# Performance work log

Measured on AMD Instinct MI355X. Metric: run time of the kernel, lower is better.

## Reference

```python
import math
import jax, jax.numpy as jnp
import numpy as np

H = 32          # num query heads
KVH = 8         # num kv heads
HD = 128        # head dim
THETA = 10000.0
ROT = HD // 2   # 64: source applies RoPE only to first head_dim//2 dims


def setup_inputs() -> dict:
    key = jax.random.key(0)
    ks = jax.random.split(key, 5)
    B, S, D = 1, 2048, 4096
    hidden_states = jax.random.normal(ks[0], (B, S, D), dtype=jnp.float32)
    # additive causal mask: 0 on/below diagonal, large negative above
    causal = jnp.tril(jnp.ones((S, S), dtype=bool))
    attention_mask = jnp.where(causal, 0.0, -1e9).astype(jnp.float32)[None, None]
    position_ids = jnp.arange(S, dtype=jnp.int32)[None, :]
    sc = 1.0 / math.sqrt(D)
    Wq = jax.random.normal(ks[1], (D, H * HD), dtype=jnp.float32) * sc
    Wk = jax.random.normal(ks[2], (D, KVH * HD), dtype=jnp.float32) * sc
    Wv = jax.random.normal(ks[3], (D, KVH * HD), dtype=jnp.float32) * sc
    Wo = jax.random.normal(ks[4], (H * HD, D), dtype=jnp.float32) * sc
    return {"hidden_states": hidden_states, "attention_mask": attention_mask,
            "position_ids": position_ids, "Wq": Wq, "Wk": Wk, "Wv": Wv, "Wo": Wo}


def _rope_cos_sin(position_ids):
    # freqs over HD (head_dim) with step 2 -> ROT=64 frequencies
    freqs = 1.0 / THETA ** (jnp.arange(0, HD, 2, dtype=jnp.float32) / HD)  # [ROT]
    # gather per position: [1, S, ROT] -> broadcast over heads
    ang = position_ids.astype(jnp.float32)[..., None] * freqs             # [1, S, ROT]
    return jnp.cos(ang)[:, None], jnp.sin(ang)[:, None]                    # [1,1,S,ROT]


def _apply_rope(x, cos, sin):
    # x: [B, h, S, HD]; rotate only first ROT dims, splitting that slice in half
    xr = x[..., :ROT]
    x1, x2 = xr[..., : ROT // 2], xr[..., ROT // 2:]
    rot = jnp.concatenate([-x2, x1], axis=-1)
    return jnp.concatenate([xr * cos + rot * sin, x[..., ROT:]], axis=-1)


def reference(hidden_states, attention_mask, position_ids, Wq, Wk, Wv, Wo):
    B, S, D = hidden_states.shape
    q = (hidden_states @ Wq).reshape(B, S, H, HD).transpose(0, 2, 1, 3)      # [B,H,S,HD]
    k = (hidden_states @ Wk).reshape(B, S, KVH, HD).transpose(0, 2, 1, 3)    # [B,KVH,S,HD]
    v = (hidden_states @ Wv).reshape(B, S, KVH, HD).transpose(0, 2, 1, 3)
    cos, sin = _rope_cos_sin(position_ids)
    q = _apply_rope(q, cos, sin)
    k = _apply_rope(k, cos, sin)
    # GQA: repeat kv heads to match query heads
    rep = H // KVH
    k = jnp.repeat(k, rep, axis=1)
    v = jnp.repeat(v, rep, axis=1)
    scores = jnp.einsum('bhqd,bhkd->bhqk', q, k) / math.sqrt(HD)
    scores = scores + attention_mask
    attn = jax.nn.softmax(scores.astype(jnp.float32), axis=-1).astype(q.dtype)
    out = jnp.einsum('bhqk,bhkd->bhqd', attn, v)                              # [B,H,S,HD]
    out = out.transpose(0, 2, 1, 3).reshape(B, S, H * HD)
    return out @ Wo
```

## Files before the change

kernel.cpp:

```cpp
#include <hip/hip_runtime.h>
#include <hip/hip_bf16.h>
#include <stdint.h>

typedef uint16_t u16;
typedef __bf16 bf16x8 __attribute__((ext_vector_type(8)));
typedef float f32x4 __attribute__((ext_vector_type(4)));
typedef u16 u16x4 __attribute__((ext_vector_type(4)));
typedef uint32_t u32x2 __attribute__((ext_vector_type(2)));

#define S_LEN 2048
#define D_MODEL 4096
#define N_HEADS 32
#define N_KVH 8
#define HEAD_DIM 128
#define QD 4096
#define KVD 1024
#define KVS 2048
#define NF  6144

#define QSC 0.1275253958595506f
#define M2F 16.0f

typedef __attribute__((address_space(3))) uint8_t lds_u8;
typedef const __attribute__((address_space(1))) uint8_t glb_u8;

__device__ __forceinline__ float bf2f(u16 x) {
    union { unsigned u; float f; } c; c.u = ((unsigned)x) << 16; return c.f;
}
__device__ __forceinline__ u16 f2bf(float f) {
    union { float f; unsigned u; } c; c.f = f;
    unsigned u = c.u;
    u += 0x7fffu + ((u >> 16) & 1u);
    return (u16)(u >> 16);
}
__device__ __forceinline__ uint32_t cvt_pk_bf16(float a, float b) {
    uint32_t r;
    asm("v_cvt_pk_bf16_f32 %0, %1, %2" : "=v"(r) : "v"(a), "v"(b));
    return r;
}

__global__ __launch_bounds__(256) void conv_f2b_kernel(
    const float* __restrict__ in, u16* __restrict__ out, int n4)
{
    int i = blockIdx.x * blockDim.x + threadIdx.x;
    if (i < n4) {
        float4 v = ((const float4*)in)[i];
        u16x4 o;
        o.x = f2bf(v.x); o.y = f2bf(v.y); o.z = f2bf(v.z); o.w = f2bf(v.w);
        ((u16x4*)out)[i] = o;
    }
}

__global__ __launch_bounds__(256) void transpose_f2b_fast(
    const float* __restrict__ in, u16* __restrict__ out, int R, int C)
{
    __shared__ u16 tile[64 * 70];
    const int cb = blockIdx.x * 64;
    const int rb = blockIdx.y * 64;
    const int t = threadIdx.x;
    const int lr = t >> 4;
    const int lc = (t & 15) * 4;
#pragma unroll
    for (int i = 0; i < 4; ++i) {
        int r = lr + i * 16;
        float4 v = *(const float4*)(in + (size_t)(rb + r) * C + cb + lc);
        u16* d = tile + r * 70 + lc;
        d[0] = f2bf(v.x); d[1] = f2bf(v.y); d[2] = f2bf(v.z); d[3] = f2bf(v.w);
    }
    __syncthreads();
    const int sc = t >> 4;
    const int sr = (t & 15) * 4;
#pragma unroll
    for (int i = 0; i < 4; ++i) {
        int c = sc + i * 16;
        u16x4 o;
        o.x = tile[(sr + 0) * 70 + c];
        o.y = tile[(sr + 1) * 70 + c];
        o.z = tile[(sr + 2) * 70 + c];
        o.w = tile[(sr + 3) * 70 + c];
        *(u16x4*)(out + (size_t)(cb + c) * R + rb + sr) = o;
    }
}

__global__ __launch_bounds__(256) void transpose_b16_fast(
    const u16* __restrict__ in, u16* __restrict__ out, int R, int C, int ld)
{
    __shared__ u16 tile[64 * 70];
    const int cb = blockIdx.x * 64;
    const int rb = blockIdx.y * 64;
    const int t = threadIdx.x;
    const int lr = t >> 4;
    const int lc = (t & 15) * 4;
#pragma unroll
    for (int i = 0; i < 4; ++i) {
        int r = lr + i * 16;
        u16x4 v = *(const u16x4*)(in + (size_t)(rb + r) * ld + cb + lc);
        u16* d = tile + r * 70 + lc;
        d[0] = v.x; d[1] = v.y; d[2] = v.z; d[3] = v.w;
    }
    __syncthreads();
    const int sc = t >> 4;
    const int sr = (t & 15) * 4;
#pragma unroll
    for (int i = 0; i < 4; ++i) {
        int c = sc + i * 16;
        u16x4 o;
        o.x = tile[(sr + 0) * 70 + c];
        o.y = tile[(sr + 1) * 70 + c];
        o.z = tile[(sr + 2) * 70 + c];
        o.w = tile[(sr + 3) * 70 + c];
        *(u16x4*)(out + (size_t)(cb + c) * R + rb + sr) = o;
    }
}

__global__ void rope_table_kernel(const int* __restrict__ pos,
                                  float* __restrict__ ctab, float* __restrict__ stab)
{
    int s = blockIdx.x;
    int i = threadIdx.x;
    float p = (float)pos[s];
    float freq = __expf(-(float)i * (9.210340371976184f / 64.0f));
    float ang = p * freq;
    ctab[s * 64 + i] = cosf(ang);
    stab[s * 64 + i] = sinf(ang);
}

#define BM 128
#define BN 128
#define BKK 64

#define GEMM_PREAMBLE(Nval)                                                    \
    const int K = D_MODEL;                                                     \
    __shared__ u16 sA[2][BM * BKK];                                            \
    __shared__ u16 sB[2][BN * BKK];                                            \
    const int nbx = (Nval) / BN;                                               \
    const int bx = blockIdx.x % nbx;                                           \
    const int by = blockIdx.x / nbx;                                           \
    const int row0 = by * BM, col0 = bx * BN;                                  \
    const int t = threadIdx.x;                                                 \
    const int w = t >> 6, l = t & 63;                                          \
    const int wr = w >> 1, wc = w & 1;                                         \
    const int l16 = l & 15, lk = l >> 4;                                       \
    f32x4 acc[4][4] = {};                                                      \
    auto stage = [&](int buf, int k0) {                                        \
        _Pragma("unroll")                                                      \
        for (int j = 0; j < 4; ++j) {                                          \
            int chunk = j * 256 + w * 64 + l;                                  \
            int r = chunk >> 3;                                                \
            int pc = chunk & 7;                                                \
            int gch = pc ^ (r & 7);                                            \
            const u16* ga = A  + (size_t)(row0 + r) * K + k0 + gch * 8;        \
            const u16* gb = BT + (size_t)(col0 + r) * K + k0 + gch * 8;        \
            __builtin_amdgcn_global_load_lds((glb_u8*)ga,                      \
                (lds_u8*)(sA[buf] + (size_t)(j * 256 + w * 64) * 8), 16, 0, 0);\
            __builtin_amdgcn_global_load_lds((glb_u8*)gb,                      \
                (lds_u8*)(sB[buf] + (size_t)(j * 256 + w * 64) * 8), 16, 0, 0);\
        }                                                                      \
    };                                                                         \
    stage(0, 0);                                                               \
    int cur = 0;                                                               \
    for (int k0 = 0; k0 < K; k0 += BKK) {                                      \
        __syncthreads();                                                       \
        if (k0 + BKK < K) stage(cur ^ 1, k0 + BKK);                            \
        const u16* cA = sA[cur];                                               \
        const u16* cB = sB[cur];                                               \
        _Pragma("unroll")                                                      \
        for (int kk = 0; kk < 2; ++kk) {                                       \
            bf16x8 af[4], bfr[4];                                              \
            _Pragma("unroll")                                                  \
            for (int m = 0; m < 4; ++m) {                                      \
                int r = wr * 64 + m * 16 + l16;                                \
                int ch = (kk * 4 + lk) ^ (r & 7);                              \
                af[m] = *(const bf16x8*)(cA + r * BKK + ch * 8);               \
            }                                                                  \
            _Pragma("unroll")                                                  \
            for (int n = 0; n < 4; ++n) {                                      \
                int r = wc * 64 + n * 16 + l16;                                \
                int ch = (kk * 4 + lk) ^ (r & 7);                              \
                bfr[n] = *(const bf16x8*)(cB + r * BKK + ch * 8);              \
            }                                                                  \
            __builtin_amdgcn_s_setprio(1);                                     \
            _Pragma("unroll")                                                  \
            for (int m = 0; m < 4; ++m)                                        \
                _Pragma("unroll")                                              \
                for (int n = 0; n < 4; ++n)                                    \
                    acc[m][n] = __builtin_amdgcn_mfma_f32_16x16x32_bf16(       \
                        af[m], bfr[n], acc[m][n], 0, 0, 0);                    \
            __builtin_amdgcn_s_setprio(0);                                     \
        }                                                                      \
        cur ^= 1;                                                              \
    }

__global__ __launch_bounds__(256) void gemm_q_kernel(
    const u16* __restrict__ A, const u16* __restrict__ BT, u16* __restrict__ Qm,
    const float* __restrict__ ctab, const float* __restrict__ stab)
{
    GEMM_PREAMBLE(QD)

    const int colbase = col0 + wc * 64;
    const bool doRot = (colbase & 127) == 0;
#pragma unroll
    for (int m = 0; m < 4; ++m) {
        const int rbase = row0 + wr * 64 + m * 16 + lk * 4;
        float vv[4][4];
#pragma unroll
        for (int n = 0; n < 4; ++n)
#pragma unroll
            for (int j = 0; j < 4; ++j) vv[n][j] = acc[m][n][j];
        if (doRot) {
#pragma unroll
            for (int n = 0; n < 2; ++n) {
                int d = n * 16 + l16;
#pragma unroll
                for (int j = 0; j < 4; ++j) {
                    int r = rbase + j;
                    float c1 = ctab[r * 64 + d],      s1 = stab[r * 64 + d];
                    float c2 = ctab[r * 64 + d + 32], s2 = stab[r * 64 + d + 32];
                    float a = vv[n][j], b = vv[n + 2][j];
                    vv[n][j]     = a * c1 - b * s1;
                    vv[n + 2][j] = b * c2 + a * s2;
                }
            }
        }
#pragma unroll
        for (int n = 0; n < 4; ++n)
#pragma unroll
            for (int j = 0; j < 4; ++j)
                Qm[(size_t)(rbase + j) * QD + colbase + n * 16 + l16] =
                    f2bf(vv[n][j] * QSC);
    }
}

__global__ __launch_bounds__(256) void gemm_kv_kernel(
    const u16* __restrict__ A, const u16* __restrict__ BT,
    u16* __restrict__ Km, u16* __restrict__ Vm,
    const float* __restrict__ ctab, const float* __restrict__ stab)
{
    GEMM_PREAMBLE(KVS)

    const int colbase = col0 + wc * 64;
    const bool isK = colbase < KVD;
    const bool doRot = isK && ((colbase & 127) == 0);
#pragma unroll
    for (int m = 0; m < 4; ++m) {
        const int rbase = row0 + wr * 64 + m * 16 + lk * 4;
        float vv[4][4];
#pragma unroll
        for (int n = 0; n < 4; ++n)
#pragma unroll
            for (int j = 0; j < 4; ++j) vv[n][j] = acc[m][n][j];
        if (doRot) {
#pragma unroll
            for (int n = 0; n < 2; ++n) {
                int d = n * 16 + l16;
#pragma unroll
                for (int j = 0; j < 4; ++j) {
                    int r = rbase + j;
                    float c1 = ctab[r * 64 + d],      s1 = stab[r * 64 + d];
                    float c2 = ctab[r * 64 + d + 32], s2 = stab[r * 64 + d + 32];
                    float a = vv[n][j], b = vv[n + 2][j];
                    vv[n][j]     = a * c1 - b * s1;
                    vv[n + 2][j] = b * c2 + a * s2;
                }
            }
        }
        if (isK) {
#pragma unroll
            for (int n = 0; n < 4; ++n)
#pragma unroll
                for (int j = 0; j < 4; ++j)
                    Km[(size_t)(rbase + j) * KVD + colbase + n * 16 + l16] =
                        f2bf(vv[n][j]);
        } else {
#pragma unroll
            for (int n = 0; n < 4; ++n)
#pragma unroll
                for (int j = 0; j < 4; ++j)
                    Vm[(size_t)(rbase + j) * KVD + (colbase - KVD) + n * 16 + l16] =
                        f2bf(vv[n][j]);
        }
    }
}

__global__ __launch_bounds__(256) void gemm_o_kernel(
    const u16* __restrict__ A, const u16* __restrict__ BT, float* __restrict__ C)
{
    GEMM_PREAMBLE(D_MODEL)

#pragma unroll
    for (int m = 0; m < 4; ++m)
#pragma unroll
        for (int n = 0; n < 4; ++n)
#pragma unroll
            for (int j = 0; j < 4; ++j) {
                int row = row0 + wr * 64 + m * 16 + lk * 4 + j;
                int col = col0 + wc * 64 + n * 16 + l16;
                C[(size_t)row * D_MODEL + col] = acc[m][n][j];
            }
}

__global__ __launch_bounds__(256) void attn_kernel(
    const u16* __restrict__ Q, const u16* __restrict__ Km, const u16* __restrict__ VT,
    u16* __restrict__ AO)
{
    const int bx = blockIdx.x;
    const int h   = bx & 31;
    const int qt  = 31 - (bx >> 5);
    const int hkv = h >> 2;
    const int t = threadIdx.x;
    const int w = t >> 6, l = t & 63;
    const int l16 = l & 15, lk = l >> 4;
    const int q0 = qt * 64 + w * 16;

    __shared__ u16 sK[2][64 * 128];
    __shared__ u16 sV[2][128 * 64];
    __shared__ u16 sP[4 * 1024];
    u16* sPw = sP + w * 1024;

    auto stageKV = [&](int buf, int kv0) {
#pragma unroll
        for (int p = 0; p < 4; ++p) {
            int P = p * 256 + w * 64 + l;
            int r = P >> 4, pc = P & 15;
            int c = ((pc & 7) ^ (r & 7)) | (pc & 8);
            const u16* g = Km + (size_t)(kv0 + r) * KVD + hkv * 128 + c * 8;
            __builtin_amdgcn_global_load_lds((glb_u8*)g,
                (lds_u8*)(sK[buf] + (size_t)(p * 256 + w * 64) * 8), 16, 0, 0);
        }
#pragma unroll
        for (int p = 0; p < 4; ++p) {
            int P = p * 256 + w * 64 + l;
            int r = P >> 3, pc = P & 7;
            int c = pc ^ (r & 7);
            const u16* g = VT + (size_t)(hkv * 128 + r) * S_LEN + kv0 + c * 8;
            __builtin_amdgcn_global_load_lds((glb_u8*)g,
                (lds_u8*)(sV[buf] + (size_t)(p * 256 + w * 64) * 8), 16, 0, 0);
        }
    };

    bf16x8 qf[4];
#pragma unroll
    for (int kk = 0; kk < 4; ++kk)
        qf[kk] = *(const bf16x8*)(Q + (size_t)(q0 + l16) * QD + h * 128 + kk * 32 + lk * 8);

    bf16x8 vones;
#pragma unroll
    for (int e = 0; e < 8; ++e) vones[e] = (__bf16)1.0f;

    f32x4 o[8] = {};
    f32x4 lacc = {};

    stageKV(0, 0);
    int cur = 0;
    for (int it = 0; it <= qt; ++it) {
        const int kv0 = it * 64;
        __syncthreads();
        if (it < qt) stageKV(cur ^ 1, kv0 + 64);
        const u16* cK = sK[cur];
        const u16* cV = sV[cur];

        f32x4 sc[4] = {};
        __builtin_amdgcn_s_setprio(1);
#pragma unroll
        for (int c = 0; c < 4; ++c)
#pragma unroll
            for (int kk = 0; kk < 4; ++kk) {
                int rk = c * 16 + l16;
                int cl = kk * 4 + lk;
                int ph = ((cl & 7) ^ (rk & 7)) | (cl & 8);
                bf16x8 kf = *(const bf16x8*)(cK + rk * 128 + ph * 8);
                sc[c] = __builtin_amdgcn_mfma_f32_16x16x32_bf16(kf, qf[kk], sc[c], 0, 0, 0);
            }
        __builtin_amdgcn_s_setprio(0);

        float p[4][4];
        if (it == qt) {
            const int qrow = q0 + l16;
#pragma unroll
            for (int c = 0; c < 4; ++c)
#pragma unroll
                for (int j = 0; j < 4; ++j) {
                    int kv = kv0 + c * 16 + lk * 4 + j;
                    float v = (kv > qrow) ? -1e30f : (sc[c][j] - M2F);
                    p[c][j] = exp2f(v);
                }
        } else {
#pragma unroll
            for (int c = 0; c < 4; ++c)
#pragma unroll
                for (int j = 0; j < 4; ++j)
                    p[c][j] = exp2f(sc[c][j] - M2F);
        }

#pragma unroll
        for (int c = 0; c < 4; ++c) {
            u32x2 val;
            val.x = cvt_pk_bf16(p[c][0], p[c][1]);
            val.y = cvt_pk_bf16(p[c][2], p[c][3]);
            int g = (2 * c + (lk >> 1)) ^ (l16 & 7);
            *(u32x2*)(sPw + l16 * 64 + g * 8 + (lk & 1) * 4) = val;
        }
        asm volatile("s_waitcnt lgkmcnt(0)" ::: "memory");
        __builtin_amdgcn_sched_barrier(0);

        bf16x8 af[2];
#pragma unroll
        for (int ks = 0; ks < 2; ++ks)
            af[ks] = *(const bf16x8*)(sPw + l16 * 64 + (((ks * 4 + lk) ^ (l16 & 7)) * 8));

        __builtin_amdgcn_s_setprio(1);
#pragma unroll
        for (int n = 0; n < 8; ++n) {
#pragma unroll
            for (int ks = 0; ks < 2; ++ks) {
                int rd = n * 16 + l16;
                int cl = ks * 4 + lk;
                int ph = cl ^ (rd & 7);
                bf16x8 vf = *(const bf16x8*)(cV + rd * 64 + ph * 8);
                o[n] = __builtin_amdgcn_mfma_f32_16x16x32_bf16(af[ks], vf, o[n], 0, 0, 0);
            }
        }
#pragma unroll
        for (int ks = 0; ks < 2; ++ks)
            lacc = __builtin_amdgcn_mfma_f32_16x16x32_bf16(af[ks], vones, lacc, 0, 0, 0);
        __builtin_amdgcn_s_setprio(0);
        cur ^= 1;
    }

    float inv[4];
#pragma unroll
    for (int j = 0; j < 4; ++j) inv[j] = __builtin_amdgcn_rcpf(lacc[j]);
#pragma unroll
    for (int n = 0; n < 8; ++n)
#pragma unroll
        for (int j = 0; j < 4; ++j) {
            int row = q0 + lk * 4 + j;
            int col = h * 128 + n * 16 + l16;
            AO[(size_t)row * QD + col] = f2bf(o[n][j] * inv[j]);
        }
}

extern "C" void kernel_launch(void* const* d_in, const int* in_sizes, int n_in,
                              void* d_out, int out_size, void* d_ws, size_t ws_size,
                              hipStream_t stream) {
    const float* X   = (const float*)d_in[0];
    const int*   pos = (const int*)d_in[2];
    const float* Wq  = (const float*)d_in[3];
    const float* Wk  = (const float*)d_in[4];
    const float* Wv  = (const float*)d_in[5];
    const float* Wo  = (const float*)d_in[6];
    float* out = (float*)d_out;

    char* ws = (char*)d_ws;
    size_t off = 0;
    auto alloc = [&](size_t bytes) -> void* {
        void* p = ws + off;
        off += (bytes + 255) & ~(size_t)255;
        return p;
    };
    u16* Xb  = (u16*)alloc((size_t)S_LEN * D_MODEL * 2);
    u16* WfT = (u16*)alloc((size_t)NF * D_MODEL * 2);
    u16* WoT = (u16*)alloc((size_t)QD * D_MODEL * 2);
    u16* Qm  = (u16*)alloc((size_t)S_LEN * QD * 2);
    u16* Km  = (u16*)alloc((size_t)S_LEN * KVD * 2);
    u16* Vm  = (u16*)alloc((size_t)S_LEN * KVD * 2);
    u16* VTm = (u16*)alloc((size_t)KVD * S_LEN * 2);
    u16* AO  = (u16*)alloc((size_t)S_LEN * QD * 2);
    float* ctab = (float*)alloc((size_t)S_LEN * 64 * 4);
    float* stab = (float*)alloc((size_t)S_LEN * 64 * 4);

    {
        int n4 = (S_LEN * D_MODEL) / 4;
        conv_f2b_kernel<<<dim3((n4 + 255) / 256), dim3(256), 0, stream>>>(X, Xb, n4);
    }

    transpose_f2b_fast<<<dim3(QD / 64, D_MODEL / 64), dim3(256), 0, stream>>>(
        Wq, WfT, D_MODEL, QD);
    transpose_f2b_fast<<<dim3(KVD / 64, D_MODEL / 64), dim3(256), 0, stream>>>(
        Wk, WfT + (size_t)QD * D_MODEL, D_MODEL, KVD);
    transpose_f2b_fast<<<dim3(KVD / 64, D_MODEL / 64), dim3(256), 0, stream>>>(
        Wv, WfT + (size_t)(QD + KVD) * D_MODEL, D_MODEL, KVD);
    transpose_f2b_fast<<<dim3(D_MODEL / 64, QD / 64), dim3(256), 0, stream>>>(
        Wo, WoT, QD, D_MODEL);

    rope_table_kernel<<<dim3(S_LEN), dim3(64), 0, stream>>>(pos, ctab, stab);

    gemm_q_kernel<<<dim3((S_LEN / BM) * (QD / BN)), dim3(256), 0, stream>>>(
        Xb, WfT, Qm, ctab, stab);
    gemm_kv_kernel<<<dim3((S_LEN / BM) * (KVS / BN)), dim3(256), 0, stream>>>(
        Xb, WfT + (size_t)QD * D_MODEL, Km, Vm, ctab, stab);

    transpose_b16_fast<<<dim3(KVD / 64, S_LEN / 64), dim3(256), 0, stream>>>(
        Vm, VTm, S_LEN, KVD, KVD);

    attn_kernel<<<dim3(32 * 32), dim3(256), 0, stream>>>(Qm, Km, VTm, AO);

    gemm_o_kernel<<<dim3((S_LEN / BM) * (D_MODEL / BN)), dim3(256), 0, stream>>>(
        AO, WoT, out);
}
```

Baseline: 334.0 us.

## Triple-buffer GEMM K-loop with BK=32 and explicit vmcnt waits

Replaces the double-buffered BK=64 LDS pipeline in the shared GEMM preamble with a three-stage BK=32 pipeline that prefetches two tiles ahead. It uses explicit s_waitcnt vmcnt plus a raw barrier instead of __syncthreads. The LDS layout is changed to pack two 32-wide rows per 64-element line with an XOR swizzle to avoid bank conflicts. The aim is to hide global-load latency better, at the cost of twice as many barriers per K and a hand-tuned wait count that must match the number of outstanding loads.

Result: slower. 379.2 us (+13.5%).

```diff
diff --git a/kernel.cpp b/kernel.cpp
--- a/kernel.cpp
+++ b/kernel.cpp
@@ -127,12 +127,13 @@
 
 #define BM 128
 #define BN 128
-#define BKK 64
+#define BKK 32
+#define NBUF 3
 
 #define GEMM_PREAMBLE(Nval)                                                    \
     const int K = D_MODEL;                                                     \
-    __shared__ u16 sA[2][BM * BKK];                                            \
-    __shared__ u16 sB[2][BN * BKK];                                            \
+    __shared__ u16 sA[NBUF][BM * BKK];                                         \
+    __shared__ u16 sB[NBUF][BN * BKK];                                         \
     const int nbx = (Nval) / BN;                                               \
     const int bx = blockIdx.x % nbx;                                           \
     const int by = blockIdx.x / nbx;                                           \
@@ -144,13 +145,14 @@
     f32x4 acc[4][4] = {};                                                      \
     auto stage = [&](int buf, int k0) {                                        \
         _Pragma("unroll")                                                      \
-        for (int j = 0; j < 4; ++j) {                                          \
-            int chunk = j * 256 + w * 64 + l;                                  \
-            int r = chunk >> 3;                                                \
-            int pc = chunk & 7;                                                \
-            int gch = pc ^ (r & 7);                                            \
-            const u16* ga = A  + (size_t)(row0 + r) * K + k0 + gch * 8;        \
-            const u16* gb = BT + (size_t)(col0 + r) * K + k0 + gch * 8;        \
+        for (int j = 0; j < 2; ++j) {                                          \
+            int C = j * 256 + w * 64 + l;                                      \
+            int rp = C >> 3;                                                   \
+            int p  = (C & 7) ^ (rp & 7);                                       \
+            int srow = rp * 2 + (p >> 2);                                      \
+            int sk   = (p & 3) * 8;                                            \
+            const u16* ga = A  + (size_t)(row0 + srow) * K + k0 + sk;          \
+            const u16* gb = BT + (size_t)(col0 + srow) * K + k0 + sk;          \
             __builtin_amdgcn_global_load_lds((glb_u8*)ga,                      \
                 (lds_u8*)(sA[buf] + (size_t)(j * 256 + w * 64) * 8), 16, 0, 0);\
             __builtin_amdgcn_global_load_lds((glb_u8*)gb,                      \
@@ -158,37 +160,41 @@
         }                                                                      \
     };                                                                         \
     stage(0, 0);                                                               \
-    int cur = 0;                                                               \
-    for (int k0 = 0; k0 < K; k0 += BKK) {                                      \
-        __syncthreads();                                                       \
-        if (k0 + BKK < K) stage(cur ^ 1, k0 + BKK);                            \
-        const u16* cA = sA[cur];                                               \
-        const u16* cB = sB[cur];                                               \
+    stage(1, BKK);                                                             \
+    const int nK = K / BKK;                                                    \
+    int bc_ = 0, bs_ = 2;                                                      \
+    for (int kt = 0; kt < nK; ++kt) {                                          \
+        if (kt + 1 < nK) { asm volatile("s_waitcnt vmcnt(4)" ::: "memory"); }  \
+        else             { asm volatile("s_waitcnt vmcnt(0)" ::: "memory"); }  \
+        __builtin_amdgcn_sched_barrier(0);                                     \
+        __builtin_amdgcn_s_barrier();                                          \
+        __builtin_amdgcn_sched_barrier(0);                                     \
+        if (kt + 2 < nK) stage(bs_, (kt + 2) * BKK);                           \
+        const u16* cA = sA[bc_];                                               \
+        const u16* cB = sB[bc_];                                               \
+        bf16x8 af[4], bfr[4];                                                  \
         _Pragma("unroll")                                                      \
-        for (int kk = 0; kk < 2; ++kk) {                                       \
-            bf16x8 af[4], bfr[4];                                              \
+        for (int m = 0; m < 4; ++m) {                                          \
+            int r = wr * 64 + m * 16 + l16;                                    \
+            af[m] = *(const bf16x8*)(cA + (r >> 1) * 64 +                      \
+                        ((((r & 1) * 4 + lk) ^ ((r >> 1) & 7)) * 8));          \
+        }                                                                      \
+        _Pragma("unroll")                                                      \
+        for (int n = 0; n < 4; ++n) {                                          \
+            int r = wc * 64 + n * 16 + l16;                                    \
+            bfr[n] = *(const bf16x8*)(cB + (r >> 1) * 64 +                     \
+                        ((((r & 1) * 4 + lk) ^ ((r >> 1) & 7)) * 8));          \
+        }                                                                      \
+        __builtin_amdgcn_s_setprio(1);                                         \
+        _Pragma("unroll")                                                      \
+        for (int m = 0; m < 4; ++m)                                            \
             _Pragma("unroll")                                                  \
-            for (int m = 0; m < 4; ++m) {                                      \
-                int r = wr * 64 + m * 16 + l16;                                \
-                int ch = (kk * 4 + lk) ^ (r & 7);                              \
-                af[m] = *(const bf16x8*)(cA + r * BKK + ch * 8);               \
-            }                                                                  \
-            _Pragma("unroll")                                                  \
-            for (int n = 0; n < 4; ++n) {                                      \
-                int r = wc * 64 + n * 16 + l16;                                \
-                int ch = (kk * 4 + lk) ^ (r & 7);                              \
-                bfr[n] = *(const bf16x8*)(cB + r * BKK + ch * 8);              \
-            }                                                                  \
-            __builtin_amdgcn_s_setprio(1);                                     \
-            _Pragma("unroll")                                                  \
-            for (int m = 0; m < 4; ++m)                                        \
-                _Pragma("unroll")                                              \
-                for (int n = 0; n < 4; ++n)                                    \
-                    acc[m][n] = __builtin_amdgcn_mfma_f32_16x16x32_bf16(       \
-                        af[m], bfr[n], acc[m][n], 0, 0, 0);                    \
-            __builtin_amdgcn_s_setprio(0);                                     \
-        }                                                                      \
-        cur ^= 1;                                                              \
+            for (int n = 0; n < 4; ++n)                                        \
+                acc[m][n] = __builtin_amdgcn_mfma_f32_16x16x32_bf16(           \
+                    af[m], bfr[n], acc[m][n], 0, 0, 0);                        \
+        __builtin_amdgcn_s_setprio(0);                                         \
+        bc_ = (bc_ == 2) ? 0 : bc_ + 1;                                        \
+        bs_ = (bs_ == 2) ? 0 : bs_ + 1;                                        \
     }
 
 __global__ __launch_bounds__(256) void gemm_q_kernel(
```
